# Kernel optimization log

Hardware: AMD Instinct MI355X
Metric: run time of the kernel (lower is better)

Reference implementation:

```python
import jax, jax.numpy as jnp
import numpy as np


def setup_inputs() -> dict:
    key = jax.random.key(0)
    k_y, k_cb = jax.random.split(key)
    B, C, H, W = 8, 192, 64, 64
    G, K = 8, 512
    d = C // G  # 24
    y = jax.random.normal(k_y, (B, C, H, W), dtype=jnp.float32)
    codebooks = jax.random.normal(k_cb, (G, K, d), dtype=jnp.float32)
    return {"y": y, "codebooks": codebooks}


def reference(y, codebooks):
    # y: [B, C, H, W]; codebooks: [G, K, d] with C == G*d
    B, C, H, W = y.shape
    G, K, d = codebooks.shape
    # split channels into G groups of dim d -> vectors at each spatial pos
    x = y.reshape(B, G, d, H, W).transpose(0, 3, 4, 1, 2)  # [B,H,W,G,d]
    x2 = jnp.sum(x * x, axis=-1, keepdims=True)            # [B,H,W,G,1]
    e2 = jnp.sum(codebooks * codebooks, axis=-1)           # [G,K]
    xe = jnp.einsum('bhwgd,gkd->bhwgk', x, codebooks)      # [B,H,W,G,K]
    dist = x2 - 2.0 * xe + e2                              # [B,H,W,G,K]
    idx = jnp.argmin(dist, axis=-1)                        # [B,H,W,G] int
    # gather quantized vectors per group (to_feather)
    q = codebooks[jnp.arange(G), idx]                      # [B,H,W,G,d]
    y_ba = q.transpose(0, 3, 4, 1, 2).reshape(B, C, H, W)  # [B,C,H,W]
    code_index = idx.transpose(0, 3, 1, 2)                 # [B,G,H,W]
    # straight-through estimator
    universal_ctx = y + jax.lax.stop_gradient(y_ba - y)
    return universal_ctx, y_ba, code_index[:, None]        # [B,1,G,H,W]
```

## Files before the change

kernel.cpp:

```cpp
#include <hip/hip_runtime.h>

#define B_   8
#define C_   192
#define HW_  4096
#define G_   8
#define K_   512
#define D_   24
#define CBSZ (K_ * D_)
#define THREADS 512
#define NBLOCKS 1024

#define FRAG_HW   12288
#define IMG_HW    13312

typedef float  f32x4 __attribute__((ext_vector_type(4)));
typedef int    i32x4 __attribute__((ext_vector_type(4)));
typedef short  s16x8 __attribute__((ext_vector_type(8)));
typedef short  s16x4 __attribute__((ext_vector_type(4)));
typedef unsigned long long u64;

static __device__ __forceinline__ unsigned umin_(unsigned a, unsigned b){return a<b?a:b;}
static __device__ __forceinline__ unsigned umax_(unsigned a, unsigned b){return a>b?a:b;}
static __device__ __forceinline__ unsigned short f2bf(float x){
    unsigned u=__float_as_uint(x);
    return (unsigned short)((u + 0x7FFFu + ((u>>16)&1u))>>16);
}

__global__ __launch_bounds__(THREADS, 8) void vq_mfma8(
    const float* __restrict__ y, const float* __restrict__ cb,
    float* __restrict__ out)
{
    __shared__ __align__(16) unsigned short sB[IMG_HW];

    const int bid = blockIdx.x;
    const int g = bid & 7;
    const int blkg = bid >> 3;
    const int tid = threadIdx.x;
    const int wave = tid >> 6, lane = tid & 63;
    const int c = lane & 15, q = lane >> 4;

    const float* cbg = cb + g * CBSZ;

    {
        const int n = tid;
        const f32x4* row4 = (const f32x4*)(cbg + n * D_);
        f32x4 rr[6];
        #pragma unroll
        for (int kb = 0; kb < 6; ++kb) rr[kb] = row4[kb];
        const int nb = (n >> 4) * 384 + (n & 15) * 8;
        #pragma unroll
        for (int kb = 0; kb < 6; ++kb) {
            const int k0 = kb * 4;
            const int off = nb + ((k0 >> 3) << 7) + (k0 & 7);
            s16x4 h;
            h[0]=(short)f2bf(rr[kb][0]); h[1]=(short)f2bf(rr[kb][1]);
            h[2]=(short)f2bf(rr[kb][2]); h[3]=(short)f2bf(rr[kb][3]);
            *(s16x4*)(&sB[off]) = h;
        }
        double s0 = 0.0, s1 = 0.0;
        #pragma unroll
        for (int kb = 0; kb < 6; ++kb) {
            double v0=(double)rr[kb][0], v1=(double)rr[kb][1];
            double v2=(double)rr[kb][2], v3=(double)rr[kb][3];
            s0 = fma(v0,v0,s0); s1 = fma(v1,v1,s1);
            s0 = fma(v2,v2,s0); s1 = fma(v3,v3,s1);
        }
        ((float*)(sB + FRAG_HW))[n] = (float)(256.0 + s0 + s1);
    }
    __syncthreads();

    float* out0 = out;
    float* out1 = out + B_*C_*HW_;
    float* out2 = out + 2*B_*C_*HW_;

    const unsigned short* aptr = sB + (lane < 48 ? lane : lane - 48) * 8;
    const f32x4* e2p = (const f32x4*)((const float*)(sB + FRAG_HW) + (q << 2));
    const unsigned qr4 = (unsigned)(q << 2);

    const int wsid  = (blkg << 3) + wave;
    const int hw    = (wsid & 255) << 4;
    const int bimg0 = wsid >> 8;
    int ybase[2];
    ybase[0] = (bimg0*C_ + g*D_)*HW_ + hw;
    ybase[1] = ybase[0] + 4*C_*HW_;

    s16x8 Xh[2], Xl[2];
    #pragma unroll
    for (int ti = 0; ti < 2; ++ti) {
        unsigned hx[4], lx[4];
        if (q < 3) {
            const float* yq = y + ybase[ti] + (q*8)*HW_ + c;
            float xf[8];
            #pragma unroll
            for (int jj = 0; jj < 8; ++jj) xf[jj] = -2.0f * yq[jj*HW_];
            #pragma unroll
            for (int p2 = 0; p2 < 4; ++p2) {
                float f0 = xf[2*p2], f1 = xf[2*p2+1];
                unsigned u0 = __float_as_uint(f0), u1v = __float_as_uint(f1);
                hx[p2] = (u1v & 0xFFFF0000u) | (u0 >> 16);
                float l0 = f0 - __uint_as_float(u0 & 0xFFFF0000u);
                float l1 = f1 - __uint_as_float(u1v & 0xFFFF0000u);
                lx[p2] = (unsigned)f2bf(l0) | ((unsigned)f2bf(l1) << 16);
            }
        } else {
            hx[0]=0u; hx[1]=0u; hx[2]=0u; hx[3]=0u;
            lx[0]=0u; lx[1]=0u; lx[2]=0u; lx[3]=0u;
        }
        Xh[ti] = __builtin_bit_cast(s16x8, (i32x4){(int)hx[0],(int)hx[1],(int)hx[2],(int)hx[3]});
        Xl[ti] = __builtin_bit_cast(s16x8, (i32x4){(int)lx[0],(int)lx[1],(int)lx[2],(int)lx[3]});
    }

    unsigned b1a[2] = {0xFFFFFFFFu, 0xFFFFFFFFu};
    unsigned b2a[2] = {0xFFFFFFFFu, 0xFFFFFFFFu};
    unsigned b3a[2] = {0xFFFFFFFFu, 0xFFFFFFFFu};
    #pragma unroll 4
    for (int t = 0; t < 32; ++t) {
        s16x8 eh  = *(const s16x8*)(aptr + t * 384);
        f32x4 e2v = e2p[t * 4];
        f32x4 a0 = __builtin_amdgcn_mfma_f32_16x16x32_bf16(eh, Xh[0], e2v, 0,0,0);
        a0       = __builtin_amdgcn_mfma_f32_16x16x32_bf16(eh, Xl[0], a0,  0,0,0);
        f32x4 a1 = __builtin_amdgcn_mfma_f32_16x16x32_bf16(eh, Xh[1], e2v, 0,0,0);
        a1       = __builtin_amdgcn_mfma_f32_16x16x32_bf16(eh, Xl[1], a1,  0,0,0);
        #pragma unroll
        for (int r = 0; r < 4; ++r) {
            const unsigned idtr = (unsigned)((t << 4) | r);
            {
                unsigned key = (__float_as_uint(a0[r]) & 0xFFFFFE00u) + idtr;
                unsigned t3, t2;
                asm("v_med3_u32 %0, %1, %2, %3" : "=v"(t3) : "v"(key), "v"(b2a[0]), "v"(b3a[0]));
                asm("v_med3_u32 %0, %1, %2, %3" : "=v"(t2) : "v"(key), "v"(b1a[0]), "v"(b2a[0]));
                b3a[0] = t3; b2a[0] = t2; b1a[0] = umin_(b1a[0], key);
            }
            {
                unsigned key = (__float_as_uint(a1[r]) & 0xFFFFFE00u) + idtr;
                unsigned t3, t2;
                asm("v_med3_u32 %0, %1, %2, %3" : "=v"(t3) : "v"(key), "v"(b2a[1]), "v"(b3a[1]));
                asm("v_med3_u32 %0, %1, %2, %3" : "=v"(t2) : "v"(key), "v"(b1a[1]), "v"(b2a[1]));
                b3a[1] = t3; b2a[1] = t2; b1a[1] = umin_(b1a[1], key);
            }
        }
    }
    #pragma unroll
    for (int ti = 0; ti < 2; ++ti) {
        b1a[ti] += qr4; b2a[ti] += qr4; b3a[ti] += qr4;
    }

    #pragma unroll
    for (int ti = 0; ti < 2; ++ti) {
        unsigned b1 = b1a[ti], b2 = b2a[ti], b3 = b3a[ti];
        #pragma unroll
        for (int d = 16; d < 64; d <<= 1) {
            unsigned o1=__shfl_xor(b1,d,64), o2=__shfl_xor(b2,d,64), o3=__shfl_xor(b3,d,64);
            unsigned x = umax_(b1,o1);
            unsigned yv= umin_(b2,o2);
            unsigned w = umax_(b2,o2);
            unsigned z = umin_(b3,o3);
            b1 = umin_(b1,o1);
            b2 = umin_(x,yv);
            b3 = umin_(umax_(x,yv), umin_(w,z));
        }

        const float v1 = __uint_as_float(b1 & 0xFFFFFE00u);
        const float v2 = __uint_as_float(b2 & 0xFFFFFE00u);
        int kwin;
        if (__ballot((v2 - v1) < 0.20f) == 0ull) {
            kwin = (int)(b1 & 511u);
        } else {
            float xfr[8];
            if (q < 3) {
                const float* yq = y + ybase[ti] + (q*8)*HW_ + c;
                #pragma unroll
                for (int jj = 0; jj < 8; ++jj) xfr[jj] = -2.0f * yq[jj*HW_];
            } else {
                #pragma unroll
                for (int jj = 0; jj < 8; ++jj) xfr[jj] = 0.0f;
            }
            double xd[8];
            #pragma unroll
            for (int jj = 0; jj < 8; ++jj) xd[jj] = (double)xfr[jj];
            const unsigned cands[3] = {b1, b2, b3};
            u64 bestk = ~0ull;
            #pragma unroll
            for (int ci = 0; ci < 3; ++ci) {
                int kc = (int)(cands[ci] & 511u);
                double s = 0.0;
                if (q < 3) {
                    const f32x4* ce4 = (const f32x4*)(cbg + kc*D_ + (q<<3));
                    float ef[8];
                    *(f32x4*)&ef[0] = ce4[0];
                    *(f32x4*)&ef[4] = ce4[1];
                    #pragma unroll
                    for (int jj = 0; jj < 8; ++jj) {
                        double ev = (double)ef[jj];
                        s = fma(ev, ev, s);
                        s = fma(xd[jj], ev, s);
                    }
                }
                s += __shfl_xor(s, 16, 64);
                s += __shfl_xor(s, 32, 64);
                s += 256.0;
                u64 kk = (((u64)__double_as_longlong(s)) & ~0x1FFull) | (u64)kc;
                bestk = kk < bestk ? kk : bestk;
            }
            kwin = (int)(bestk & 511ull);
        }

        const float* cw = cbg + kwin * D_;
        if (q < 3) {
            const f32x4* cw4 = (const f32x4*)(cw + (q<<3));
            float v[8];
            *(f32x4*)&v[0] = cw4[0];
            *(f32x4*)&v[4] = cw4[1];
            const int ob = ybase[ti] + (q*8)*HW_ + c;
            #pragma unroll
            for (int jj = 0; jj < 8; ++jj) {
                out0[ob + jj*HW_] = v[jj];
                out1[ob + jj*HW_] = v[jj];
            }
        }
        if (lane < 16) {
            const int bimg = bimg0 + ti*4;
            out2[(bimg*G_ + g)*HW_ + hw + lane] = (float)kwin;
        }
    }
}

extern "C" void kernel_launch(void* const* d_in, const int* in_sizes, int n_in,
                              void* d_out, int out_size, void* d_ws, size_t ws_size,
                              hipStream_t stream) {
    const float* y  = (const float*)d_in[0];
    const float* cb = (const float*)d_in[1];
    float* out = (float*)d_out;
    (void)d_ws; (void)ws_size;

    vq_mfma8<<<dim3(NBLOCKS), dim3(THREADS), 0, stream>>>(y, cb, out);
}
```

Baseline: 115.3 us.

## Precompute bf16 codebook images in staging kernel, add low-part MFMA term, halve grid

New measurement: 113.9 us. Within noise of the previous version (-1.2%).

```diff
diff --git a/kernel.cpp b/kernel.cpp
--- a/kernel.cpp
+++ b/kernel.cpp
@@ -8,10 +8,15 @@
 #define D_   24
 #define CBSZ (K_ * D_)
 #define THREADS 512
-#define NBLOCKS 1024
-
-#define FRAG_HW   12288
-#define IMG_HW    13312
+#define NBLOCKS 512
+
+#define FRAG_HW    12288
+#define E2_OFF_HW  12288
+#define EL_OFF_HW  13312
+#define IMG_HW     25600
+#define WS_IMG_HW  13312
+#define WS_EL_BASE (8 * WS_IMG_HW)
+#define WS_BIG_BYTES ((8 * WS_IMG_HW + 8 * FRAG_HW) * 2)
 
 typedef float  f32x4 __attribute__((ext_vector_type(4)));
 typedef int    i32x4 __attribute__((ext_vector_type(4)));
@@ -25,10 +30,55 @@
     unsigned u=__float_as_uint(x);
     return (unsigned short)((u + 0x7FFFu + ((u>>16)&1u))>>16);
 }
-
-__global__ __launch_bounds__(THREADS, 8) void vq_mfma8(
+static __device__ __forceinline__ float bf2f(unsigned short h){return __uint_as_float(((unsigned)h)<<16);}
+static __device__ __forceinline__ int dec_id(unsigned idb){
+    return (int)((idb & 0x1F0u) | ((idb & 3u) << 2) | ((idb >> 2) & 3u));
+}
+
+__global__ __launch_bounds__(256) void vq_stage(
+    const float* __restrict__ cb, unsigned short* __restrict__ ws, int wr_el)
+{
+    const int g = blockIdx.x >> 3;
+    const int s = blockIdx.x & 7;
+    const int tid = threadIdx.x;
+    const float* cbg = cb + g * CBSZ;
+    unsigned short* img = ws + g * WS_IMG_HW;
+    unsigned short* eli = ws + WS_EL_BASE + g * FRAG_HW;
+
+    for (int i = tid; i < 384; i += 256) {
+        int gi = s * 384 + i;
+        f32x4 v = ((const f32x4*)cbg)[gi];
+        int i4 = gi << 2;
+        int n  = i4 / 24;
+        int k0 = i4 - n * 24;
+        int off = (n >> 4) * 384 + (((k0 >> 3) << 4) + (n & 15)) * 8 + (k0 & 7);
+        s16x4 h, l;
+        #pragma unroll
+        for (int j = 0; j < 4; ++j) {
+            unsigned short eh = f2bf(v[j]);
+            h[j] = (short)eh;
+            l[j] = (short)f2bf(v[j] - bf2f(eh));
+        }
+        *(s16x4*)(&img[off]) = h;
+        if (wr_el) *(s16x4*)(&eli[off]) = l;
+    }
+    if (tid < 64) {
+        int n = s * 64 + tid;
+        const float* row = cbg + n * D_;
+        double s0 = 0.0, s1 = 0.0;
+        #pragma unroll
+        for (int j = 0; j < D_; j += 2) {
+            double v0 = (double)row[j], v1 = (double)row[j+1];
+            s0 = fma(v0,v0,s0); s1 = fma(v1,v1,s1);
+        }
+        ((float*)(img + E2_OFF_HW))[n] = (float)(256.0 + s0 + s1);
+    }
+}
+
+template<bool ELWS>
+__global__ __launch_bounds__(THREADS, 4) void vq_main(
     const float* __restrict__ y, const float* __restrict__ cb,
-    float* __restrict__ out)
+    const unsigned short* __restrict__ ws, float* __restrict__ out)
 {
     __shared__ __align__(16) unsigned short sB[IMG_HW];
 
@@ -42,30 +92,40 @@
     const float* cbg = cb + g * CBSZ;
 
     {
-        const int n = tid;
-        const f32x4* row4 = (const f32x4*)(cbg + n * D_);
-        f32x4 rr[6];
-        #pragma unroll
-        for (int kb = 0; kb < 6; ++kb) rr[kb] = row4[kb];
-        const int nb = (n >> 4) * 384 + (n & 15) * 8;
-        #pragma unroll
-        for (int kb = 0; kb < 6; ++kb) {
-            const int k0 = kb * 4;
-            const int off = nb + ((k0 >> 3) << 7) + (k0 & 7);
-            s16x4 h;
-            h[0]=(short)f2bf(rr[kb][0]); h[1]=(short)f2bf(rr[kb][1]);
-            h[2]=(short)f2bf(rr[kb][2]); h[3]=(short)f2bf(rr[kb][3]);
-            *(s16x4*)(&sB[off]) = h;
-        }
-        double s0 = 0.0, s1 = 0.0;
-        #pragma unroll
-        for (int kb = 0; kb < 6; ++kb) {
-            double v0=(double)rr[kb][0], v1=(double)rr[kb][1];
-            double v2=(double)rr[kb][2], v3=(double)rr[kb][3];
-            s0 = fma(v0,v0,s0); s1 = fma(v1,v1,s1);
-            s0 = fma(v2,v2,s0); s1 = fma(v3,v3,s1);
-        }
-        ((float*)(sB + FRAG_HW))[n] = (float)(256.0 + s0 + s1);
+        const char* src = (const char*)(ws + g * WS_IMG_HW);
+        char* dst = (char*)sB;
+        #pragma unroll
+        for (int it = 0; it < 4; ++it) {
+            int off = it * 8192 + tid * 16;
+            if (off < 26624)
+                *(i32x4*)(dst + off) = *(const i32x4*)(src + off);
+        }
+    }
+    if (ELWS) {
+        const char* src = (const char*)(ws + WS_EL_BASE + g * FRAG_HW);
+        char* dst = (char*)(sB + EL_OFF_HW);
+        #pragma unroll
+        for (int it = 0; it < 3; ++it) {
+            int off = it * 8192 + tid * 16;
+            *(i32x4*)(dst + off) = *(const i32x4*)(src + off);
+        }
+    } else {
+        #pragma unroll
+        for (int it = 0; it < 6; ++it) {
+            int gi = it * THREADS + tid;
+            f32x4 v = ((const f32x4*)cbg)[gi];
+            int i4 = gi << 2;
+            int n  = i4 / 24;
+            int k0 = i4 - n * 24;
+            int off = (n >> 4) * 384 + (((k0 >> 3) << 4) + (n & 15)) * 8 + (k0 & 7);
+            s16x4 l;
+            #pragma unroll
+            for (int j = 0; j < 4; ++j) {
+                unsigned short eh = f2bf(v[j]);
+                l[j] = (short)f2bf(v[j] - bf2f(eh));
+            }
+            *(s16x4*)(&sB[EL_OFF_HW + off]) = l;
+        }
     }
     __syncthreads();
 
@@ -73,154 +133,157 @@
     float* out1 = out + B_*C_*HW_;
     float* out2 = out + 2*B_*C_*HW_;
 
-    const unsigned short* aptr = sB + (lane < 48 ? lane : lane - 48) * 8;
-    const f32x4* e2p = (const f32x4*)((const float*)(sB + FRAG_HW) + (q << 2));
-    const unsigned qr4 = (unsigned)(q << 2);
-
-    const int wsid  = (blkg << 3) + wave;
-    const int hw    = (wsid & 255) << 4;
-    const int bimg0 = wsid >> 8;
-    int ybase[2];
-    ybase[0] = (bimg0*C_ + g*D_)*HW_ + hw;
-    ybase[1] = ybase[0] + 4*C_*HW_;
-
-    s16x8 Xh[2], Xl[2];
-    #pragma unroll
-    for (int ti = 0; ti < 2; ++ti) {
-        unsigned hx[4], lx[4];
-        if (q < 3) {
-            const float* yq = y + ybase[ti] + (q*8)*HW_ + c;
-            float xf[8];
-            #pragma unroll
-            for (int jj = 0; jj < 8; ++jj) xf[jj] = -2.0f * yq[jj*HW_];
-            #pragma unroll
-            for (int p2 = 0; p2 < 4; ++p2) {
-                float f0 = xf[2*p2], f1 = xf[2*p2+1];
-                unsigned u0 = __float_as_uint(f0), u1v = __float_as_uint(f1);
-                hx[p2] = (u1v & 0xFFFF0000u) | (u0 >> 16);
-                float l0 = f0 - __uint_as_float(u0 & 0xFFFF0000u);
-                float l1 = f1 - __uint_as_float(u1v & 0xFFFF0000u);
-                lx[p2] = (unsigned)f2bf(l0) | ((unsigned)f2bf(l1) << 16);
-            }
-        } else {
-            hx[0]=0u; hx[1]=0u; hx[2]=0u; hx[3]=0u;
-            lx[0]=0u; lx[1]=0u; lx[2]=0u; lx[3]=0u;
-        }
-        Xh[ti] = __builtin_bit_cast(s16x8, (i32x4){(int)hx[0],(int)hx[1],(int)hx[2],(int)hx[3]});
-        Xl[ti] = __builtin_bit_cast(s16x8, (i32x4){(int)lx[0],(int)lx[1],(int)lx[2],(int)lx[3]});
-    }
-
-    unsigned b1a[2] = {0xFFFFFFFFu, 0xFFFFFFFFu};
-    unsigned b2a[2] = {0xFFFFFFFFu, 0xFFFFFFFFu};
-    unsigned b3a[2] = {0xFFFFFFFFu, 0xFFFFFFFFu};
-    #pragma unroll 4
-    for (int t = 0; t < 32; ++t) {
-        s16x8 eh  = *(const s16x8*)(aptr + t * 384);
-        f32x4 e2v = e2p[t * 4];
-        f32x4 a0 = __builtin_amdgcn_mfma_f32_16x16x32_bf16(eh, Xh[0], e2v, 0,0,0);
-        a0       = __builtin_amdgcn_mfma_f32_16x16x32_bf16(eh, Xl[0], a0,  0,0,0);
-        f32x4 a1 = __builtin_amdgcn_mfma_f32_16x16x32_bf16(eh, Xh[1], e2v, 0,0,0);
-        a1       = __builtin_amdgcn_mfma_f32_16x16x32_bf16(eh, Xl[1], a1,  0,0,0);
-        #pragma unroll
-        for (int r = 0; r < 4; ++r) {
-            const unsigned idtr = (unsigned)((t << 4) | r);
-            {
-                unsigned key = (__float_as_uint(a0[r]) & 0xFFFFFE00u) + idtr;
-                unsigned t3, t2;
-                asm("v_med3_u32 %0, %1, %2, %3" : "=v"(t3) : "v"(key), "v"(b2a[0]), "v"(b3a[0]));
-                asm("v_med3_u32 %0, %1, %2, %3" : "=v"(t2) : "v"(key), "v"(b1a[0]), "v"(b2a[0]));
-                b3a[0] = t3; b2a[0] = t2; b1a[0] = umin_(b1a[0], key);
-            }
-            {
-                unsigned key = (__float_as_uint(a1[r]) & 0xFFFFFE00u) + idtr;
-                unsigned t3, t2;
-                asm("v_med3_u32 %0, %1, %2, %3" : "=v"(t3) : "v"(key), "v"(b2a[1]), "v"(b3a[1]));
-                asm("v_med3_u32 %0, %1, %2, %3" : "=v"(t2) : "v"(key), "v"(b1a[1]), "v"(b2a[1]));
-                b3a[1] = t3; b2a[1] = t2; b1a[1] = umin_(b1a[1], key);
-            }
-        }
-    }
-    #pragma unroll
-    for (int ti = 0; ti < 2; ++ti) {
-        b1a[ti] += qr4; b2a[ti] += qr4; b3a[ti] += qr4;
-    }
-
-    #pragma unroll
-    for (int ti = 0; ti < 2; ++ti) {
-        unsigned b1 = b1a[ti], b2 = b2a[ti], b3 = b3a[ti];
-        #pragma unroll
-        for (int d = 16; d < 64; d <<= 1) {
-            unsigned o1=__shfl_xor(b1,d,64), o2=__shfl_xor(b2,d,64), o3=__shfl_xor(b3,d,64);
-            unsigned x = umax_(b1,o1);
-            unsigned yv= umin_(b2,o2);
-            unsigned w = umax_(b2,o2);
-            unsigned z = umin_(b3,o3);
-            b1 = umin_(b1,o1);
-            b2 = umin_(x,yv);
-            b3 = umin_(umax_(x,yv), umin_(w,z));
-        }
-
-        const float v1 = __uint_as_float(b1 & 0xFFFFFE00u);
-        const float v2 = __uint_as_float(b2 & 0xFFFFFE00u);
-        int kwin;
-        if (__ballot((v2 - v1) < 0.20f) == 0ull) {
-            kwin = (int)(b1 & 511u);
-        } else {
-            float xfr[8];
+    const unsigned short* aH = sB + (lane < 48 ? lane : lane - 48) * 8;
+    const unsigned short* aL = aH + EL_OFF_HW;
+    const f32x4* e2p = (const f32x4*)((const float*)(sB + E2_OFF_HW) + (q << 2));
+
+    const int wsid = (blkg << 3) + wave;
+
+    #pragma unroll 1
+    for (int p = 0; p < 2; ++p) {
+        const int tt0   = wsid + (p << 10);
+        const int hw    = (tt0 & 255) << 4;
+        const int bimg0 = tt0 >> 8;
+        int ybase[2];
+        ybase[0] = (bimg0*C_ + g*D_)*HW_ + hw;
+        ybase[1] = ybase[0] + 2*C_*HW_;
+
+        s16x8 Xh[2], Xl[2];
+        #pragma unroll
+        for (int ti = 0; ti < 2; ++ti) {
+            unsigned hx[4], lx[4];
             if (q < 3) {
                 const float* yq = y + ybase[ti] + (q*8)*HW_ + c;
-                #pragma unroll
-                for (int jj = 0; jj < 8; ++jj) xfr[jj] = -2.0f * yq[jj*HW_];
+                float xf[8];
+                #pragma unroll
+                for (int jj = 0; jj < 8; ++jj) xf[jj] = -2.0f * yq[jj*HW_];
+                #pragma unroll
+                for (int p2 = 0; p2 < 4; ++p2) {
+                    float f0 = xf[2*p2], f1 = xf[2*p2+1];
+                    unsigned u0 = __float_as_uint(f0), u1v = __float_as_uint(f1);
+                    hx[p2] = (u1v & 0xFFFF0000u) | (u0 >> 16);
+                    float l0 = f0 - __uint_as_float(u0 & 0xFFFF0000u);
+                    float l1 = f1 - __uint_as_float(u1v & 0xFFFF0000u);
+                    lx[p2] = (unsigned)f2bf(l0) | ((unsigned)f2bf(l1) << 16);
+                }
             } else {
-                #pragma unroll
-                for (int jj = 0; jj < 8; ++jj) xfr[jj] = 0.0f;
-            }
-            double xd[8];
+                hx[0]=0u; hx[1]=0u; hx[2]=0u; hx[3]=0u;
+                lx[0]=0u; lx[1]=0u; lx[2]=0u; lx[3]=0u;
+            }
+            Xh[ti] = __builtin_bit_cast(s16x8, (i32x4){(int)hx[0],(int)hx[1],(int)hx[2],(int)hx[3]});
+            Xl[ti] = __builtin_bit_cast(s16x8, (i32x4){(int)lx[0],(int)lx[1],(int)lx[2],(int)lx[3]});
+        }
+
+        unsigned b1a[2] = {~0u, ~0u}, b2a[2] = {~0u, ~0u}, b3a[2] = {~0u, ~0u};
+        #pragma unroll 4
+        for (int t = 0; t < 32; ++t) {
+            s16x8 eh  = *(const s16x8*)(aH + t * 384);
+            s16x8 el  = *(const s16x8*)(aL + t * 384);
+            f32x4 e2v = e2p[t * 4];
+            f32x4 a0 = __builtin_amdgcn_mfma_f32_16x16x32_bf16(eh, Xh[0], e2v, 0,0,0);
+            a0       = __builtin_amdgcn_mfma_f32_16x16x32_bf16(eh, Xl[0], a0,  0,0,0);
+            a0       = __builtin_amdgcn_mfma_f32_16x16x32_bf16(el, Xh[0], a0,  0,0,0);
+            f32x4 a1 = __builtin_amdgcn_mfma_f32_16x16x32_bf16(eh, Xh[1], e2v, 0,0,0);
+            a1       = __builtin_amdgcn_mfma_f32_16x16x32_bf16(eh, Xl[1], a1,  0,0,0);
+            a1       = __builtin_amdgcn_mfma_f32_16x16x32_bf16(el, Xh[1], a1,  0,0,0);
             #pragma unroll
-            for (int jj = 0; jj < 8; ++jj) xd[jj] = (double)xfr[jj];
-            const unsigned cands[3] = {b1, b2, b3};
-            u64 bestk = ~0ull;
+            for (int r = 0; r < 4; ++r) {
+                const unsigned id7 = (unsigned)((t << 2) | r);
+                {
+                    unsigned key = (__float_as_uint(a0[r]) & 0xFFFFFF80u) + id7;
+                    unsigned t3, t2;
+                    asm("v_med3_u32 %0, %1, %2, %3" : "=v"(t3) : "v"(key), "v"(b2a[0]), "v"(b3a[0]));
+                    asm("v_med3_u32 %0, %1, %2, %3" : "=v"(t2) : "v"(key), "v"(b1a[0]), "v"(b2a[0]));
+                    b3a[0] = t3; b2a[0] = t2; b1a[0] = umin_(b1a[0], key);
+                }
+                {
+                    unsigned key = (__float_as_uint(a1[r]) & 0xFFFFFF80u) + id7;
+                    unsigned t3, t2;
+                    asm("v_med3_u32 %0, %1, %2, %3" : "=v"(t3) : "v"(key), "v"(b2a[1]), "v"(b3a[1]));
+                    asm("v_med3_u32 %0, %1, %2, %3" : "=v"(t2) : "v"(key), "v"(b1a[1]), "v"(b2a[1]));
+                    b3a[1] = t3; b2a[1] = t2; b1a[1] = umin_(b1a[1], key);
+                }
+            }
+        }
+
+        #pragma unroll
+        for (int ti = 0; ti < 2; ++ti) {
+            unsigned b1 = (b1a[ti] << 2) | (unsigned)q;
+            unsigned b2 = (b2a[ti] << 2) | (unsigned)q;
+            unsigned b3 = (b3a[ti] << 2) | (unsigned)q;
             #pragma unroll
-            for (int ci = 0; ci < 3; ++ci) {
-                int kc = (int)(cands[ci] & 511u);
-                double s = 0.0;
+            for (int d = 16; d < 64; d <<= 1) {
+                unsigned o1=__shfl_xor(b1,d,64), o2=__shfl_xor(b2,d,64), o3=__shfl_xor(b3,d,64);
+                unsigned x = umax_(b1,o1);
+                unsigned yv= umin_(b2,o2);
+                unsigned w = umax_(b2,o2);
+                unsigned z = umin_(b3,o3);
+                b1 = umin_(b1,o1);
+                b2 = umin_(x,yv);
+                b3 = umin_(umax_(x,yv), umin_(w,z));
+            }
+
+            const int gap = (int)((b2 >> 9) - (b1 >> 9));
+            int kwin;
+            if (__ballot(gap < 8) == 0ull) {
+                kwin = dec_id(b1 & 511u);
+            } else {
+                float xfr[8];
                 if (q < 3) {
-                    const f32x4* ce4 = (const f32x4*)(cbg + kc*D_ + (q<<3));
-                    float ef[8];
-                    *(f32x4*)&ef[0] = ce4[0];
-                    *(f32x4*)&ef[4] = ce4[1];
+                    const float* yq = y + ybase[ti] + (q*8)*HW_ + c;
                     #pragma unroll
-                    for (int jj = 0; jj < 8; ++jj) {
-                        double ev = (double)ef[jj];
-                        s = fma(ev, ev, s);
-                        s = fma(xd[jj], ev, s);
+                    for (int jj = 0; jj < 8; ++jj) xfr[jj] = -2.0f * yq[jj*HW_];
+                } else {
+                    #pragma unroll
+                    for (int jj = 0; jj < 8; ++jj) xfr[jj] = 0.0f;
+                }
+                double xd[8];
+                #pragma unroll
+                for (int jj = 0; jj < 8; ++jj) xd[jj] = (double)xfr[jj];
+                const unsigned cands[3] = {b1, b2, b3};
+                u64 bestk = ~0ull;
+                #pragma unroll
+                for (int ci = 0; ci < 3; ++ci) {
+                    int kc = dec_id(cands[ci] & 511u);
+                    double s = 0.0;
+                    if (q < 3) {
+                        const f32x4* ce4 = (const f32x4*)(cbg + kc*D_ + (q<<3));
+                        float ef[8];
+                        *(f32x4*)&ef[0] = ce4[0];
+                        *(f32x4*)&ef[4] = ce4[1];
+                        #pragma unroll
+                        for (int jj = 0; jj < 8; ++jj) {
+                            double ev = (double)ef[jj];
+                            s = fma(ev, ev, s);
+                            s = fma(xd[jj], ev, s);
+                        }
                     }
-                }
-                s += __shfl_xor(s, 16, 64);
-                s += __shfl_xor(s, 32, 64);
-                s += 256.0;
-                u64 kk = (((u64)__double_as_longlong(s)) & ~0x1FFull) | (u64)kc;
-                bestk = kk < bestk ? kk : bestk;
-            }
-            kwin = (int)(bestk & 511ull);
-        }
-
-        const float* cw = cbg + kwin * D_;
-        if (q < 3) {
-            const f32x4* cw4 = (const f32x4*)(cw + (q<<3));
-            float v[8];
-            *(f32x4*)&v[0] = cw4[0];
-            *(f32x4*)&v[4] = cw4[1];
-            const int ob = ybase[ti] + (q*8)*HW_ + c;
-            #pragma unroll
-            for (int jj = 0; jj < 8; ++jj) {
-                out0[ob + jj*HW_] = v[jj];
-                out1[ob + jj*HW_] = v[jj];
-            }
-        }
-        if (lane < 16) {
-            const int bimg = bimg0 + ti*4;
-            out2[(bimg*G_ + g)*HW_ + hw + lane] = (float)kwin;
+                    s += __shfl_xor(s, 16, 64);
+                    s += __shfl_xor(s, 32, 64);
+                    s += 256.0;
+                    u64 kk = (((u64)__double_as_longlong(s)) & ~0x1FFull) | (u64)kc;
+                    bestk = kk < bestk ? kk : bestk;
+                }
+                kwin = (int)(bestk & 511ull);
+            }
+
+            const float* cw = cbg + kwin * D_;
+            if (q < 3) {
+                const f32x4* cw4 = (const f32x4*)(cw + (q<<3));
+                float v[8];
+                *(f32x4*)&v[0] = cw4[0];
+                *(f32x4*)&v[4] = cw4[1];
+                const int ob = ybase[ti] + (q*8)*HW_ + c;
+                #pragma unroll
+                for (int jj = 0; jj < 8; ++jj) {
+                    out0[ob + jj*HW_] = v[jj];
+                    out1[ob + jj*HW_] = v[jj];
+                }
+            }
+            if (lane < 16) {
+                const int bimg = bimg0 + 2*ti;
+                out2[(bimg*G_ + g)*HW_ + hw + lane] = (float)kwin;
+            }
         }
     }
 }
@@ -231,7 +294,10 @@
     const float* y  = (const float*)d_in[0];
     const float* cb = (const float*)d_in[1];
     float* out = (float*)d_out;
-    (void)d_ws; (void)ws_size;
-
-    vq_mfma8<<<dim3(NBLOCKS), dim3(THREADS), 0, stream>>>(y, cb, out);
-}
+    unsigned short* ws = (unsigned short*)d_ws;
+
+    const bool big = ws_size >= (size_t)WS_BIG_BYTES;
+    vq_stage<<<dim3(64), dim3(256), 0, stream>>>(cb, ws, big ? 1 : 0);
+    if (big) vq_main<true ><<<dim3(NBLOCKS), dim3(THREADS), 0, stream>>>(y, cb, ws, out);
+    else     vq_main<false><<<dim3(NBLOCKS), dim3(THREADS), 0, stream>>>(y, cb, ws, out);
+}
```
